# Performance work log

Measured on AMD Instinct MI355X. Metric: run time of the kernel, lower is better.

## Reference

```python
import jax, jax.numpy as jnp
import numpy as np

TEMPERATURE = 1.0
BIG = 1e30  # sentinel for masked min/max
NEG = -1e30  # masked logit


def _masked_log_softmax(x, m):
    # m: bool mask [B, N]; rows with no valid entries are handled by the caller
    return jax.nn.log_softmax(jnp.where(m, x, NEG), axis=-1)


def setup_inputs() -> dict:
    key = jax.random.key(0)
    k1, k2, k3 = jax.random.split(key, 3)
    B, N = 4096, 6000
    y_pred = jax.random.normal(k1, (B, N), dtype=jnp.float32)
    y_true = jax.random.normal(k2, (B, N), dtype=jnp.float32) * 0.05  # daily returns scale
    masks = jax.random.randint(k3, (B, N), 0, 2, dtype=jnp.int32)
    return {"y_pred": y_pred, "y_true": y_true, "masks": masks}


def reference(y_pred, y_true, masks):
    m = masks > 0  # [B, N] bool
    mf = m.astype(y_pred.dtype)
    n = mf.sum(-1)  # [B] number of valid stocks per day
    valid = n >= 2  # rows with <2 valid entries are skipped (contribute 0)

    # min-max normalize y_true over valid entries (label_smoothing == 0)
    t_min = jnp.min(jnp.where(m, y_true, BIG), axis=-1, keepdims=True)
    t_max = jnp.max(jnp.where(m, y_true, -BIG), axis=-1, keepdims=True)
    rng = t_max - t_min
    true_norm = jnp.where(rng > 0, (y_true - t_min) / (rng + 1e-12), y_true)

    logp_pred = _masked_log_softmax(y_pred / TEMPERATURE, m)
    logp_true = _masked_log_softmax(true_norm / TEMPERATURE, m)
    p_true = jnp.exp(logp_true)

    # F.kl_div(pred_prob.log(), true_prob, reduction='batchmean') on a 1-D
    # vector of length n divides the summed KL by n.
    kl_elem = jnp.where(m, p_true * (logp_true - logp_pred), 0.0)
    kl = kl_elem.sum(-1) / jnp.maximum(n, 1.0)  # [B]

    batch_size = y_pred.shape[0]
    return jnp.sum(jnp.where(valid, kl, 0.0)) / batch_size
```

## Files before the change

### kernel.cpp

```cpp
#include <hip/hip_runtime.h>
#include <math.h>

#define NCOL  6000
#define NV    1500
#define BLOCK 512
#define NWAVE 8

__device__ __forceinline__ float wave_max_f(float v) {
    #pragma unroll
    for (int off = 32; off > 0; off >>= 1) v = fmaxf(v, __shfl_xor(v, off, 64));
    return v;
}
__device__ __forceinline__ float wave_min_f(float v) {
    #pragma unroll
    for (int off = 32; off > 0; off >>= 1) v = fminf(v, __shfl_xor(v, off, 64));
    return v;
}
__device__ __forceinline__ int wave_sum_i(int v) {
    #pragma unroll
    for (int off = 32; off > 0; off >>= 1) v += __shfl_xor(v, off, 64);
    return v;
}
__device__ __forceinline__ double wave_sum_d(double v) {
    #pragma unroll
    for (int off = 32; off > 0; off >>= 1) v += __shfl_xor(v, off, 64);
    return v;
}

__global__ __launch_bounds__(BLOCK) void row_kl_kernel(
    const float* __restrict__ yp, const float* __restrict__ yt,
    const int* __restrict__ mk, float* __restrict__ rowkl)
{
    __shared__ float sp[NCOL];
    __shared__ float st[NCOL];
    __shared__ float swf[3][NWAVE];
    __shared__ int   swi[NWAVE];
    __shared__ double swd[3][NWAVE];

    const int row  = blockIdx.x;
    const int tid  = threadIdx.x;
    const int lane = tid & 63;
    const int wid  = tid >> 6;

    const float4* yp4 = reinterpret_cast<const float4*>(yp) + (size_t)row * NV;
    const float4* yt4 = reinterpret_cast<const float4*>(yt) + (size_t)row * NV;
    const int4*   mk4 = reinterpret_cast<const int4*>(mk) + (size_t)row * NV;

    float maxp = -1e30f, tmin = 1e30f, tmax = -1e30f;
    int cnt = 0;

    for (int v = tid; v < NV; v += BLOCK) {
        float4 xp = yp4[v];
        float4 xt = yt4[v];
        int4   mm = mk4[v];
        const int e = 4 * v;
        {
            bool m = mm.x > 0;
            float x = m ? xp.x : -1e30f;
            float t = m ? xt.x : -1e30f;
            sp[e + 0] = x; st[e + 0] = t;
            maxp = fmaxf(maxp, x);
            tmax = fmaxf(tmax, t);
            tmin = fminf(tmin, m ? xt.x : 1e30f);
            cnt += m;
        }
        {
            bool m = mm.y > 0;
            float x = m ? xp.y : -1e30f;
            float t = m ? xt.y : -1e30f;
            sp[e + 1] = x; st[e + 1] = t;
            maxp = fmaxf(maxp, x);
            tmax = fmaxf(tmax, t);
            tmin = fminf(tmin, m ? xt.y : 1e30f);
            cnt += m;
        }
        {
            bool m = mm.z > 0;
            float x = m ? xp.z : -1e30f;
            float t = m ? xt.z : -1e30f;
            sp[e + 2] = x; st[e + 2] = t;
            maxp = fmaxf(maxp, x);
            tmax = fmaxf(tmax, t);
            tmin = fminf(tmin, m ? xt.z : 1e30f);
            cnt += m;
        }
        {
            bool m = mm.w > 0;
            float x = m ? xp.w : -1e30f;
            float t = m ? xt.w : -1e30f;
            sp[e + 3] = x; st[e + 3] = t;
            maxp = fmaxf(maxp, x);
            tmax = fmaxf(tmax, t);
            tmin = fminf(tmin, m ? xt.w : 1e30f);
            cnt += m;
        }
    }

    maxp = wave_max_f(maxp);
    tmin = wave_min_f(tmin);
    tmax = wave_max_f(tmax);
    cnt  = wave_sum_i(cnt);
    __syncthreads();
    if (lane == 0) { swf[0][wid] = maxp; swf[1][wid] = tmin; swf[2][wid] = tmax; swi[wid] = cnt; }
    __syncthreads();
    maxp = -1e30f; tmin = 1e30f; tmax = -1e30f; cnt = 0;
    #pragma unroll
    for (int j = 0; j < NWAVE; ++j) {
        maxp = fmaxf(maxp, swf[0][j]);
        tmin = fminf(tmin, swf[1][j]);
        tmax = fmaxf(tmax, swf[2][j]);
        cnt += swi[j];
    }

    const float rng   = tmax - tmin;
    const bool scaled = rng > 0.0f;
    const float inv_s = 1.0f / (rng + 1e-12f);
    const float maxz  = scaled ? rng * inv_s : tmax;

    double Zp = 0.0, S1 = 0.0, S2 = 0.0;
    for (int i = tid; i < NCOL; i += BLOCK) {
        float x = sp[i];
        float t = st[i];
        float ep = __expf(x - maxp);
        float z  = scaled ? (t - tmin) * inv_s : t;
        z = fmaxf(z, -1e30f);
        float e1 = __expf(z - maxz);
        Zp += (double)ep;
        S1 += (double)e1;
        S2 += (double)e1 * (double)(z - x);
    }
    Zp = wave_sum_d(Zp);
    S1 = wave_sum_d(S1);
    S2 = wave_sum_d(S2);
    if (lane == 0) { swd[0][wid] = Zp; swd[1][wid] = S1; swd[2][wid] = S2; }
    __syncthreads();
    if (tid == 0) {
        double zp = 0.0, s1 = 0.0, s2 = 0.0;
        #pragma unroll
        for (int j = 0; j < NWAVE; ++j) { zp += swd[0][j]; s1 += swd[1][j]; s2 += swd[2][j]; }
        float val = 0.0f;
        if (cnt >= 2) {
            double kl = s2 / s1 + ((double)maxp + log(zp) - (double)maxz - log(s1));
            double v  = kl / (double)cnt;
            if (isfinite(v)) val = (float)v;
        }
        rowkl[row] = val;
    }
}

__global__ __launch_bounds__(256) void final_reduce_kernel(
    const float* __restrict__ rowkl, float* __restrict__ out, int nrows)
{
    __shared__ double swd[4];
    const int tid  = threadIdx.x;
    const int lane = tid & 63;
    const int wid  = tid >> 6;
    double acc = 0.0;
    for (int i = tid; i < nrows; i += 256) acc += (double)rowkl[i];
    acc = wave_sum_d(acc);
    if (lane == 0) swd[wid] = acc;
    __syncthreads();
    if (tid == 0) {
        double tot = 0.0;
        #pragma unroll
        for (int j = 0; j < 4; ++j) tot += swd[j];
        out[0] = (float)(tot / (double)nrows);
    }
}

extern "C" void kernel_launch(void* const* d_in, const int* in_sizes, int n_in,
                              void* d_out, int out_size, void* d_ws, size_t ws_size,
                              hipStream_t stream) {
    const float* y_pred = (const float*)d_in[0];
    const float* y_true = (const float*)d_in[1];
    const int*   masks  = (const int*)d_in[2];
    float* out = (float*)d_out;
    float* rowkl = (float*)d_ws;

    const int B = in_sizes[0] / NCOL;

    row_kl_kernel<<<B, BLOCK, 0, stream>>>(y_pred, y_true, masks, rowkl);
    final_reduce_kernel<<<1, 256, 0, stream>>>(rowkl, out, B);
}
```

Baseline: 61.69 us.

## Keep per-thread row data in registers and issue all global loads upfront

All global loads for a thread's three float4 chunks are issued before any computation, so more memory requests are in flight at once. The masked prediction values stay in registers across the reduction instead of passing through shared memory, and only the target values are staged in a float4 shared buffer. Padded lanes are handled by clamping the load index and zeroing the mask. This adds register pressure, and the launch-bounds occupancy hint could cause spills. It also removes one barrier.

```diff
diff --git a/kernel.cpp b/kernel.cpp
--- a/kernel.cpp
+++ b/kernel.cpp
@@ -5,6 +5,7 @@
 #define NV    1500
 #define BLOCK 512
 #define NWAVE 8
+#define EPT   3
 
 __device__ __forceinline__ float wave_max_f(float v) {
     #pragma unroll
@@ -27,14 +28,13 @@
     return v;
 }
 
-__global__ __launch_bounds__(BLOCK) void row_kl_kernel(
+__global__ __launch_bounds__(BLOCK, 8) void row_kl_kernel(
     const float* __restrict__ yp, const float* __restrict__ yt,
     const int* __restrict__ mk, float* __restrict__ rowkl)
 {
-    __shared__ float sp[NCOL];
-    __shared__ float st[NCOL];
-    __shared__ float swf[3][NWAVE];
-    __shared__ int   swi[NWAVE];
+    __shared__ float4 st4[EPT * BLOCK];
+    __shared__ float  swf[3][NWAVE];
+    __shared__ int    swi[NWAVE];
     __shared__ double swd[3][NWAVE];
 
     const int row  = blockIdx.x;
@@ -46,61 +46,66 @@
     const float4* yt4 = reinterpret_cast<const float4*>(yt) + (size_t)row * NV;
     const int4*   mk4 = reinterpret_cast<const int4*>(mk) + (size_t)row * NV;
 
+    float4 xp[EPT], xt[EPT];
+    int4   mm[EPT];
+    #pragma unroll
+    for (int j = 0; j < EPT; ++j) {
+        const int v  = tid + j * BLOCK;
+        const int vc = (v < NV) ? v : 0;
+        xp[j] = yp4[vc];
+        xt[j] = yt4[vc];
+        mm[j] = mk4[vc];
+    }
+    if (tid + (EPT - 1) * BLOCK >= NV) {
+        mm[EPT - 1].x = 0; mm[EPT - 1].y = 0; mm[EPT - 1].z = 0; mm[EPT - 1].w = 0;
+    }
+
+    float xm[4 * EPT];
     float maxp = -1e30f, tmin = 1e30f, tmax = -1e30f;
     int cnt = 0;
 
-    for (int v = tid; v < NV; v += BLOCK) {
-        float4 xp = yp4[v];
-        float4 xt = yt4[v];
-        int4   mm = mk4[v];
-        const int e = 4 * v;
+    #pragma unroll
+    for (int j = 0; j < EPT; ++j) {
+        float4 tq;
         {
-            bool m = mm.x > 0;
-            float x = m ? xp.x : -1e30f;
-            float t = m ? xt.x : -1e30f;
-            sp[e + 0] = x; st[e + 0] = t;
-            maxp = fmaxf(maxp, x);
-            tmax = fmaxf(tmax, t);
-            tmin = fminf(tmin, m ? xt.x : 1e30f);
-            cnt += m;
+            bool m = mm[j].x > 0;
+            float x = m ? xp[j].x : -1e30f;
+            float t = m ? xt[j].x : -1e30f;
+            xm[4 * j + 0] = x; tq.x = t;
+            maxp = fmaxf(maxp, x); tmax = fmaxf(tmax, t);
+            tmin = fminf(tmin, m ? xt[j].x : 1e30f); cnt += m;
         }
         {
-            bool m = mm.y > 0;
-            float x = m ? xp.y : -1e30f;
-            float t = m ? xt.y : -1e30f;
-            sp[e + 1] = x; st[e + 1] = t;
-            maxp = fmaxf(maxp, x);
-            tmax = fmaxf(tmax, t);
-            tmin = fminf(tmin, m ? xt.y : 1e30f);
-            cnt += m;
+            bool m = mm[j].y > 0;
+            float x = m ? xp[j].y : -1e30f;
+            float t = m ? xt[j].y : -1e30f;
+            xm[4 * j + 1] = x; tq.y = t;
+            maxp = fmaxf(maxp, x); tmax = fmaxf(tmax, t);
+            tmin = fminf(tmin, m ? xt[j].y : 1e30f); cnt += m;
         }
         {
-            bool m = mm.z > 0;
-            float x = m ? xp.z : -1e30f;
-            float t = m ? xt.z : -1e30f;
-            sp[e + 2] = x; st[e + 2] = t;
-            maxp = fmaxf(maxp, x);
-            tmax = fmaxf(tmax, t);
-            tmin = fminf(tmin, m ? xt.z : 1e30f);
-            cnt += m;
+            bool m = mm[j].z > 0;
+            float x = m ? xp[j].z : -1e30f;
+            float t = m ? xt[j].z : -1e30f;
+            xm[4 * j + 2] = x; tq.z = t;
+            maxp = fmaxf(maxp, x); tmax = fmaxf(tmax, t);
+            tmin = fminf(tmin, m ? xt[j].z : 1e30f); cnt += m;
         }
         {
-            bool m = mm.w > 0;
-            float x = m ? xp.w : -1e30f;
-            float t = m ? xt.w : -1e30f;
-            sp[e + 3] = x; st[e + 3] = t;
-            maxp = fmaxf(maxp, x);
-            tmax = fmaxf(tmax, t);
-            tmin = fminf(tmin, m ? xt.w : 1e30f);
-            cnt += m;
+            bool m = mm[j].w > 0;
+            float x = m ? xp[j].w : -1e30f;
+            float t = m ? xt[j].w : -1e30f;
+            xm[4 * j + 3] = x; tq.w = t;
+            maxp = fmaxf(maxp, x); tmax = fmaxf(tmax, t);
+            tmin = fminf(tmin, m ? xt[j].w : 1e30f); cnt += m;
         }
+        st4[tid + j * BLOCK] = tq;
     }
 
     maxp = wave_max_f(maxp);
     tmin = wave_min_f(tmin);
     tmax = wave_max_f(tmax);
     cnt  = wave_sum_i(cnt);
-    __syncthreads();
     if (lane == 0) { swf[0][wid] = maxp; swf[1][wid] = tmin; swf[2][wid] = tmax; swi[wid] = cnt; }
     __syncthreads();
     maxp = -1e30f; tmin = 1e30f; tmax = -1e30f; cnt = 0;
@@ -118,16 +123,21 @@
     const float maxz  = scaled ? rng * inv_s : tmax;
 
     double Zp = 0.0, S1 = 0.0, S2 = 0.0;
-    for (int i = tid; i < NCOL; i += BLOCK) {
-        float x = sp[i];
-        float t = st[i];
-        float ep = __expf(x - maxp);
-        float z  = scaled ? (t - tmin) * inv_s : t;
-        z = fmaxf(z, -1e30f);
-        float e1 = __expf(z - maxz);
-        Zp += (double)ep;
-        S1 += (double)e1;
-        S2 += (double)e1 * (double)(z - x);
+    #pragma unroll
+    for (int j = 0; j < EPT; ++j) {
+        float4 tq = st4[tid + j * BLOCK];
+        #pragma unroll
+        for (int c = 0; c < 4; ++c) {
+            float x = xm[4 * j + c];
+            float t = (c == 0) ? tq.x : (c == 1) ? tq.y : (c == 2) ? tq.z : tq.w;
+            float ep = __expf(x - maxp);
+            float z  = scaled ? (t - tmin) * inv_s : t;
+            z = fmaxf(z, -1e30f);
+            float e1 = __expf(z - maxz);
+            Zp += (double)ep;
+            S1 += (double)e1;
+            S2 += (double)e1 * (double)(z - x);
+        }
     }
     Zp = wave_sum_d(Zp);
     S1 = wave_sum_d(S1);
```

Result: faster. 57.46 us (-6.8%).
